# Kernel optimization log

Hardware: AMD Instinct MI355X
Metric: run time of the kernel (lower is better)

The kernel has to match this reference:

```python
import jax, jax.numpy as jnp
import numpy as np

B, T, C, H = 4, 4096, 768, 64  # batch, seq, embed_size, head_size


def setup_inputs() -> dict:
    key = jax.random.key(0)
    kx, kq, kk, kv = jax.random.split(key, 4)
    s = 1.0 / np.sqrt(C)
    return {
        "x": jax.random.normal(kx, (B, T, C), dtype=jnp.float32),
        "Wq": jax.random.normal(kq, (C, H), dtype=jnp.float32) * s,
        "Wk": jax.random.normal(kk, (C, H), dtype=jnp.float32) * s,
        "Wv": jax.random.normal(kv, (C, H), dtype=jnp.float32) * s,
    }


def reference(x, Wq, Wk, Wv):
    Bx, Tx, Cx = x.shape
    Q = x @ Wq  # [B, T, H]
    K = x @ Wk
    V = x @ Wv
    # NOTE: original scales by sqrt(C) = sqrt(embed_size), not head_size
    scores = jnp.einsum('bqh,bkh->bqk', Q, K) / jnp.sqrt(jnp.asarray(Cx, x.dtype))
    causal = jnp.tril(jnp.ones((Tx, Tx), dtype=bool))
    scores = jnp.where(causal, scores, -jnp.inf)
    weights = jax.nn.softmax(scores, axis=-1)
    # dropout = identity in eval mode
    return jnp.einsum('bqk,bkh->bqh', weights, V)
```

## Files before the change

kernel.cpp:

```cpp
#include <hip/hip_runtime.h>

typedef __bf16 bf16x8 __attribute__((ext_vector_type(8)));
typedef float f32x4 __attribute__((ext_vector_type(4)));
typedef short s16x4 __attribute__((ext_vector_type(4)));

#define MFMA16(a,b,c)    __builtin_amdgcn_mfma_f32_16x16x32_bf16(a,b,c,0,0,0)
#define MFMA16K16(a,b,c) __builtin_amdgcn_mfma_f32_16x16x16bf16_1k(a,b,c,0,0,0)

__device__ __forceinline__ unsigned short f2b(float x){
  __bf16 b = (__bf16)x;
  return __builtin_bit_cast(unsigned short, b);
}
__device__ __forceinline__ float b2f(unsigned short u){
  return __builtin_bit_cast(float, ((unsigned)u)<<16);
}

__device__ __forceinline__ void gld16(const void* g, void* l){
  __builtin_amdgcn_global_load_lds(
      (const __attribute__((address_space(1))) unsigned int*)g,
      (__attribute__((address_space(3))) unsigned int*)l, 16, 0, 0);
}

__global__ __launch_bounds__(256) void pack_w(const float* __restrict__ Wq,
                                              const float* __restrict__ Wk,
                                              const float* __restrict__ Wv,
                                              unsigned short* __restrict__ Wt){
  int idx = blockIdx.x*256 + threadIdx.x;
  int n = idx/768, c = idx - n*768;
  const float* W = (n < 64) ? Wq : ((n < 128) ? Wk : Wv);
  Wt[n*768 + c] = f2b(W[c*64 + (n & 63)]);
}

__global__ __launch_bounds__(256,2) void qkv_proj(const float* __restrict__ x,
                                                  const unsigned short* __restrict__ Wt,
                                                  unsigned short* __restrict__ Qb,
                                                  unsigned short* __restrict__ Kb,
                                                  unsigned short* __restrict__ Vt){
  __shared__ __attribute__((aligned(16))) float Xl[2][32*64];
  __shared__ __attribute__((aligned(16))) unsigned short Wl[2][192*64];
  const int tid = threadIdx.x;
  const int w = tid>>6, l = tid&63, quad = l>>4, lr = l&15;
  const int row0 = blockIdx.x*32;

  auto stage = [&](int kk, int buf){
#pragma unroll
    for(int i=0;i<2;i++){
      int n = (w*2+i)*4 + (l>>4);
      int sc = (l&15) ^ (n&15);
      gld16(x + (size_t)(row0+n)*768 + kk*64 + sc*4, &Xl[buf][(w*2+i)*256]);
    }
#pragma unroll
    for(int i=0;i<6;i++){
      int gr0 = (w*6+i)*8;
      int n = gr0 + (l>>3);
      int sc = (l&7) ^ (l>>3);
      gld16(Wt + (size_t)n*768 + kk*64 + sc*8, &Wl[buf][gr0*64]);
    }
  };

  f32x4 acc[2][3];
#pragma unroll
  for(int mt=0;mt<2;mt++)
#pragma unroll
    for(int nt=0;nt<3;nt++) acc[mt][nt] = (f32x4)0.0f;

  stage(0, 0);
  int buf = 0;
  for(int kk=0; kk<12; kk++){
    __syncthreads();
    if(kk+1 < 12) stage(kk+1, buf^1);
    bf16x8 a[2][2];
#pragma unroll
    for(int mt=0;mt<2;mt++){
#pragma unroll
      for(int ks=0;ks<2;ks++){
        int c = ks*8 + quad*2;
        f32x4 v0 = *(const f32x4*)&Xl[buf][(mt*16+lr)*64 + ((c   ^ lr)&15)*4];
        f32x4 v1 = *(const f32x4*)&Xl[buf][(mt*16+lr)*64 + (((c+1)^ lr)&15)*4];
#pragma unroll
        for(int jj=0;jj<4;jj++){ a[mt][ks][jj] = (__bf16)v0[jj]; a[mt][ks][4+jj] = (__bf16)v1[jj]; }
      }
    }
#pragma unroll
    for(int nt=0;nt<3;nt++){
#pragma unroll
      for(int ks=0;ks<2;ks++){
        int n = w*48 + nt*16 + lr;
        int q = ks*4 + quad;
        bf16x8 bfr = *(const bf16x8*)&Wl[buf][n*64 + ((q ^ (lr&7))&7)*8];
#pragma unroll
        for(int mt=0;mt<2;mt++) acc[mt][nt] = MFMA16(a[mt][ks], bfr, acc[mt][nt]);
      }
    }
    buf ^= 1;
  }
  const int b_ = row0>>12;
  const float sc = 0.03608439182435161f;
#pragma unroll
  for(int mt=0;mt<2;mt++){
    const int t0 = (row0 & 4095) + mt*16 + quad*4;
#pragma unroll
    for(int nt=0;nt<3;nt++){
      int g = w*48 + nt*16 + lr;
      if(g < 64){
#pragma unroll
        for(int r=0;r<4;r++) Qb[((size_t)(b_*4096 + t0 + r))*64 + g] = f2b(acc[mt][nt][r]*sc);
      } else if(g < 128){
#pragma unroll
        for(int r=0;r<4;r++) Kb[((size_t)(b_*4096 + t0 + r))*64 + (g-64)] = f2b(acc[mt][nt][r]);
      } else {
        ushort4 pk;
        pk.x = f2b(acc[mt][nt][0]); pk.y = f2b(acc[mt][nt][1]);
        pk.z = f2b(acc[mt][nt][2]); pk.w = f2b(acc[mt][nt][3]);
        *(ushort4*)&Vt[((size_t)(b_*64 + (g-128)))*4096 + t0] = pk;
      }
    }
  }
}

__device__ __forceinline__ void attn_stage(const unsigned short* kbp, const unsigned short* vbp,
                                           int kt, int w, int r8, int cj,
                                           unsigned short* Kl, unsigned short* Vl){
#pragma unroll
  for(int i=0;i<2;i++){
    int row = w*16 + i*8 + r8;
    int gc = cj ^ r8;
    gld16(kbp + ((size_t)(kt*64 + row))*64 + gc*8, Kl + (w*16 + i*8)*64);
    gld16(vbp + ((size_t)row)*4096 + kt*64 + gc*8, Vl + (w*16 + i*8)*64);
  }
}

__global__ __launch_bounds__(256,2) void attn(const unsigned short* __restrict__ Qb,
                                              const unsigned short* __restrict__ Kb,
                                              const unsigned short* __restrict__ Vt,
                                              unsigned short* __restrict__ Opart,
                                              float* __restrict__ Rpart){
  __shared__ __attribute__((aligned(16))) unsigned short Kl[2][64*64];
  __shared__ __attribute__((aligned(16))) unsigned short Vl[2][64*64];
  const int tid = threadIdx.x;
  const int w = tid>>6, l = tid&63, quad = l>>4, lr = l&15;
  const int xx = 271 - blockIdx.x;
  int i = 0, accu = 0;
  while(true){ int c = (i+2)>>1; if(accu + c > xx) break; accu += c; i++; }
  const int r = xx - accu;
  const int b = blockIdx.y;
  const int q0 = i*128;
  const int lo = r*4;
  const int hi = min(lo+4, 2*i+2);
  const int diag0 = 2*i;
  const int r8 = l>>3, cj = l&7;
  const int lx = lr & 7;
  bf16x8 aq[2][2];
#pragma unroll
  for(int m=0;m<2;m++){
    const unsigned short* qp = Qb + ((size_t)(b*4096 + q0 + w*32 + m*16 + lr))*64 + quad*8;
    aq[m][0] = *(const bf16x8*)qp;
    aq[m][1] = *(const bf16x8*)(qp + 32);
  }
  f32x4 o_[2][4];
#pragma unroll
  for(int m=0;m<2;m++)
#pragma unroll
    for(int nt=0;nt<4;nt++) o_[m][nt] = (f32x4)0.0f;
  float rs[2] = {0.f, 0.f};
  const unsigned short* kbp = Kb + ((size_t)b*4096)*64;
  const unsigned short* vbp = Vt + ((size_t)b*64)*4096;

  attn_stage(kbp, vbp, lo, w, r8, cj, Kl[0], Vl[0]);
  int cur = 0;
  for(int kt = lo; kt < hi; kt++){
    __syncthreads();
    if(kt+1 < hi) attn_stage(kbp, vbp, kt+1, w, r8, cj, Kl[cur^1], Vl[cur^1]);
    f32x4 s4[2][4];
#pragma unroll
    for(int ct=0;ct<4;ct++){
      int base = (ct*16+lr)*64;
      bf16x8 b0 = *(const bf16x8*)&Kl[cur][base + ((quad    ^ lx)<<3)];
      bf16x8 b1 = *(const bf16x8*)&Kl[cur][base + (((4+quad)^ lx)<<3)];
#pragma unroll
      for(int m=0;m<2;m++){
        f32x4 z = (f32x4)0.0f;
        z = MFMA16(b0, aq[m][0], z);
        s4[m][ct] = MFMA16(b1, aq[m][1], z);
      }
    }
    s16x4 bp[2][4];
    if(kt >= diag0){
#pragma unroll
      for(int m=0;m<2;m++){
        int qg = q0 + w*32 + m*16 + lr;
#pragma unroll
        for(int ct=0;ct<4;ct++){
          float p[4];
#pragma unroll
          for(int rr=0;rr<4;rr++){
            int kg = kt*64 + ct*16 + quad*4 + rr;
            p[rr] = (kg <= qg) ? __expf(s4[m][ct][rr]) : 0.0f;
            rs[m] += p[rr];
          }
          int2 pk;
          pk.x = (int)((unsigned)f2b(p[0]) | ((unsigned)f2b(p[1])<<16));
          pk.y = (int)((unsigned)f2b(p[2]) | ((unsigned)f2b(p[3])<<16));
          bp[m][ct] = __builtin_bit_cast(s16x4, pk);
        }
      }
    } else {
#pragma unroll
      for(int m=0;m<2;m++){
#pragma unroll
        for(int ct=0;ct<4;ct++){
          float p[4];
#pragma unroll
          for(int rr=0;rr<4;rr++){
            p[rr] = __expf(s4[m][ct][rr]);
            rs[m] += p[rr];
          }
          int2 pk;
          pk.x = (int)((unsigned)f2b(p[0]) | ((unsigned)f2b(p[1])<<16));
          pk.y = (int)((unsigned)f2b(p[2]) | ((unsigned)f2b(p[3])<<16));
          bp[m][ct] = __builtin_bit_cast(s16x4, pk);
        }
      }
    }
#pragma unroll
    for(int ct=0;ct<4;ct++){
#pragma unroll
      for(int nt=0;nt<4;nt++){
        s16x4 av = *(const s16x4*)&Vl[cur][(nt*16+lr)*64
                      + (((ct*2 + (quad>>1)) ^ lx)<<3) + (quad&1)*4];
#pragma unroll
        for(int m=0;m<2;m++) o_[m][nt] = MFMA16K16(av, bp[m][ct], o_[m][nt]);
      }
    }
    cur ^= 1;
  }
  const int slab = r*4 + b;
#pragma unroll
  for(int m=0;m<2;m++){
    float t = rs[m];
    t += __shfl_xor(t, 16, 64);
    t += __shfl_xor(t, 32, 64);
    int row = q0 + w*32 + m*16 + lr;
    if(quad == 0) Rpart[slab*4096 + row] = t;
#pragma unroll
    for(int nt=0;nt<4;nt++){
      ushort4 pk;
      pk.x = f2b(o_[m][nt][0]); pk.y = f2b(o_[m][nt][1]);
      pk.z = f2b(o_[m][nt][2]); pk.w = f2b(o_[m][nt][3]);
      *(ushort4*)&Opart[((size_t)(slab*4096 + row))*64 + nt*16 + quad*4] = pk;
    }
  }
}

__global__ __launch_bounds__(256) void combine(const unsigned short* __restrict__ Opart,
                                               const float* __restrict__ Rpart,
                                               float* __restrict__ out){
  int gid = blockIdx.x*256 + threadIdx.x;
  int cg = gid & 15;
  int t  = (gid >> 4) & 4095;
  int b  = gid >> 16;
  int i  = t >> 7;
  int np = (i + 2) >> 1;
  float o0=0.f, o1=0.f, o2=0.f, o3=0.f, rsum=0.f;
  for(int r=0; r<np; r++){
    int slab = r*4 + b;
    rsum += Rpart[slab*4096 + t];
    ushort4 u = *(const ushort4*)(Opart + ((size_t)(slab*4096 + t))*64 + cg*4);
    o0 += b2f(u.x); o1 += b2f(u.y); o2 += b2f(u.z); o3 += b2f(u.w);
  }
  float inv = 1.0f/rsum;
  f32x4 v; v[0]=o0*inv; v[1]=o1*inv; v[2]=o2*inv; v[3]=o3*inv;
  *(f32x4*)(out + ((size_t)(b*4096 + t))*64 + cg*4) = v;
}

extern "C" void kernel_launch(void* const* d_in, const int* in_sizes, int n_in,
                              void* d_out, int out_size, void* d_ws, size_t ws_size,
                              hipStream_t stream){
  const float* x  = (const float*)d_in[0];
  const float* Wq = (const float*)d_in[1];
  const float* Wk = (const float*)d_in[2];
  const float* Wv = (const float*)d_in[3];
  float* out = (float*)d_out;
  char* ws = (char*)d_ws;
  unsigned short* Wt = (unsigned short*)(ws);
  unsigned short* Qb = (unsigned short*)(ws + 0x080000);
  unsigned short* Kb = (unsigned short*)(ws + 0x280000);
  unsigned short* Vt = (unsigned short*)(ws + 0x480000);
  unsigned short* Opart = (unsigned short*)(ws + 0x680000);
  float* Rpart = (float*)(ws + 0x2680000);
  hipLaunchKernelGGL(pack_w,   dim3(576),     dim3(256), 0, stream, Wq, Wk, Wv, Wt);
  hipLaunchKernelGGL(qkv_proj, dim3(512),     dim3(256), 0, stream, x, Wt, Qb, Kb, Vt);
  hipLaunchKernelGGL(attn,     dim3(272, 4),  dim3(256), 0, stream, Qb, Kb, Vt, Opart, Rpart);
  hipLaunchKernelGGL(combine,  dim3(1024),    dim3(256), 0, stream, Opart, Rpart, out);
}
```

Before: 131.0 us.

## Split QKV projection output columns across two blocks and raise occupancy bounds

The QKV projection grid gains a second dimension that splits the 192 output columns into two 96-column halves, with each wave computing a 16x48 tile instead of 32x48. This doubles the block count, shrinks the shared-memory weight buffer and the accumulator registers, and launch bounds are raised to allow more blocks per CU. The aim is to spread the projection over more CUs and hide latency better. The cost is that each x tile is now loaded from global memory twice, once per half. The attention kernel's launch-bounds minimum is also raised from 2 to 3 blocks, which may tighten register allocation and cause spills.

```diff
diff --git a/kernel.cpp b/kernel.cpp
--- a/kernel.cpp
+++ b/kernel.cpp
@@ -31,16 +31,19 @@
   Wt[n*768 + c] = f2b(W[c*64 + (n & 63)]);
 }
 
-__global__ __launch_bounds__(256,2) void qkv_proj(const float* __restrict__ x,
+__global__ __launch_bounds__(256,4) void qkv_proj(const float* __restrict__ x,
                                                   const unsigned short* __restrict__ Wt,
                                                   unsigned short* __restrict__ Qb,
                                                   unsigned short* __restrict__ Kb,
                                                   unsigned short* __restrict__ Vt){
   __shared__ __attribute__((aligned(16))) float Xl[2][32*64];
-  __shared__ __attribute__((aligned(16))) unsigned short Wl[2][192*64];
+  __shared__ __attribute__((aligned(16))) unsigned short Wl[2][96*64];
   const int tid = threadIdx.x;
   const int w = tid>>6, l = tid&63, quad = l>>4, lr = l&15;
   const int row0 = blockIdx.x*32;
+  const int ch = blockIdx.y;
+  const int wr = w & 1;
+  const int wc = w >> 1;
 
   auto stage = [&](int kk, int buf){
 #pragma unroll
@@ -50,70 +53,61 @@
       gld16(x + (size_t)(row0+n)*768 + kk*64 + sc*4, &Xl[buf][(w*2+i)*256]);
     }
 #pragma unroll
-    for(int i=0;i<6;i++){
-      int gr0 = (w*6+i)*8;
+    for(int i=0;i<3;i++){
+      int gr0 = (w*3+i)*8;
       int n = gr0 + (l>>3);
       int sc = (l&7) ^ (l>>3);
-      gld16(Wt + (size_t)n*768 + kk*64 + sc*8, &Wl[buf][gr0*64]);
+      gld16(Wt + (size_t)(ch*96 + n)*768 + kk*64 + sc*8, &Wl[buf][gr0*64]);
     }
   };
 
-  f32x4 acc[2][3];
-#pragma unroll
-  for(int mt=0;mt<2;mt++)
-#pragma unroll
-    for(int nt=0;nt<3;nt++) acc[mt][nt] = (f32x4)0.0f;
+  f32x4 acc[3];
+#pragma unroll
+  for(int nt=0;nt<3;nt++) acc[nt] = (f32x4)0.0f;
 
   stage(0, 0);
   int buf = 0;
   for(int kk=0; kk<12; kk++){
     __syncthreads();
     if(kk+1 < 12) stage(kk+1, buf^1);
-    bf16x8 a[2][2];
-#pragma unroll
-    for(int mt=0;mt<2;mt++){
+    bf16x8 a[2];
+#pragma unroll
+    for(int ks=0;ks<2;ks++){
+      int c = ks*8 + quad*2;
+      f32x4 v0 = *(const f32x4*)&Xl[buf][(wr*16+lr)*64 + ((c    ^ lr)&15)*4];
+      f32x4 v1 = *(const f32x4*)&Xl[buf][(wr*16+lr)*64 + (((c+1)^ lr)&15)*4];
+#pragma unroll
+      for(int jj=0;jj<4;jj++){ a[ks][jj] = (__bf16)v0[jj]; a[ks][4+jj] = (__bf16)v1[jj]; }
+    }
+#pragma unroll
+    for(int nt=0;nt<3;nt++){
 #pragma unroll
       for(int ks=0;ks<2;ks++){
-        int c = ks*8 + quad*2;
-        f32x4 v0 = *(const f32x4*)&Xl[buf][(mt*16+lr)*64 + ((c   ^ lr)&15)*4];
-        f32x4 v1 = *(const f32x4*)&Xl[buf][(mt*16+lr)*64 + (((c+1)^ lr)&15)*4];
-#pragma unroll
-        for(int jj=0;jj<4;jj++){ a[mt][ks][jj] = (__bf16)v0[jj]; a[mt][ks][4+jj] = (__bf16)v1[jj]; }
-      }
-    }
-#pragma unroll
-    for(int nt=0;nt<3;nt++){
-#pragma unroll
-      for(int ks=0;ks<2;ks++){
-        int n = w*48 + nt*16 + lr;
+        int n = wc*48 + nt*16 + lr;
         int q = ks*4 + quad;
         bf16x8 bfr = *(const bf16x8*)&Wl[buf][n*64 + ((q ^ (lr&7))&7)*8];
-#pragma unroll
-        for(int mt=0;mt<2;mt++) acc[mt][nt] = MFMA16(a[mt][ks], bfr, acc[mt][nt]);
+        acc[nt] = MFMA16(a[ks], bfr, acc[nt]);
       }
     }
     buf ^= 1;
   }
   const int b_ = row0>>12;
+  const int t0 = (row0 & 4095) + wr*16 + quad*4;
   const float sc = 0.03608439182435161f;
 #pragma unroll
-  for(int mt=0;mt<2;mt++){
-    const int t0 = (row0 & 4095) + mt*16 + quad*4;
-#pragma unroll
-    for(int nt=0;nt<3;nt++){
-      int g = w*48 + nt*16 + lr;
-      if(g < 64){
-#pragma unroll
-        for(int r=0;r<4;r++) Qb[((size_t)(b_*4096 + t0 + r))*64 + g] = f2b(acc[mt][nt][r]*sc);
-      } else if(g < 128){
-#pragma unroll
-        for(int r=0;r<4;r++) Kb[((size_t)(b_*4096 + t0 + r))*64 + (g-64)] = f2b(acc[mt][nt][r]);
-      } else {
-        ushort4 pk;
-        pk.x = f2b(acc[mt][nt][0]); pk.y = f2b(acc[mt][nt][1]);
-        pk.z = f2b(acc[mt][nt][2]); pk.w = f2b(acc[mt][nt][3]);
-        *(ushort4*)&Vt[((size_t)(b_*64 + (g-128)))*4096 + t0] = pk;
-      }
+  for(int nt=0;nt<3;nt++){
+    int g = ch*96 + wc*48 + nt*16 + lr;
+    if(g < 64){
+#pragma unroll
+      for(int r=0;r<4;r++) Qb[((size_t)(b_*4096 + t0 + r))*64 + g] = f2b(acc[nt][r]*sc);
+    } else if(g < 128){
+#pragma unroll
+      for(int r=0;r<4;r++) Kb[((size_t)(b_*4096 + t0 + r))*64 + (g-64)] = f2b(acc[nt][r]);
+    } else {
+      ushort4 pk;
+      pk.x = f2b(acc[nt][0]); pk.y = f2b(acc[nt][1]);
+      pk.z = f2b(acc[nt][2]); pk.w = f2b(acc[nt][3]);
+      *(ushort4*)&Vt[((size_t)(b_*64 + (g-128)))*4096 + t0] = pk;
     }
   }
 }
@@ -130,7 +124,7 @@
   }
 }
 
-__global__ __launch_bounds__(256,2) void attn(const unsigned short* __restrict__ Qb,
+__global__ __launch_bounds__(256,3) void attn(const unsigned short* __restrict__ Qb,
                                               const unsigned short* __restrict__ Kb,
                                               const unsigned short* __restrict__ Vt,
                                               unsigned short* __restrict__ Opart,
@@ -289,7 +283,7 @@
   unsigned short* Opart = (unsigned short*)(ws + 0x680000);
   float* Rpart = (float*)(ws + 0x2680000);
   hipLaunchKernelGGL(pack_w,   dim3(576),     dim3(256), 0, stream, Wq, Wk, Wv, Wt);
-  hipLaunchKernelGGL(qkv_proj, dim3(512),     dim3(256), 0, stream, x, Wt, Qb, Kb, Vt);
+  hipLaunchKernelGGL(qkv_proj, dim3(512, 2),  dim3(256), 0, stream, x, Wt, Qb, Kb, Vt);
   hipLaunchKernelGGL(attn,     dim3(272, 4),  dim3(256), 0, stream, Qb, Kb, Vt, Opart, Rpart);
   hipLaunchKernelGGL(combine,  dim3(1024),    dim3(256), 0, stream, Opart, Rpart, out);
 }
```

New measurement: 131.9 us. No clear change (+0.7%).
